# Performance work log

Measured on AMD Instinct MI355X. Metric: run time of the kernel, lower is better.

The kernel has to match this reference:

```python
import jax, jax.numpy as jnp
import numpy as np

APPERTURE = 256
Q_SCALE = 0.06


def setup_inputs() -> dict:
    key = jax.random.key(0)
    ks = jax.random.split(key, 5)
    B, N, D_IN, D_OUT = 4, 4096, 1024, 1024
    std = 1.0 / np.sqrt(D_IN)
    x = jax.random.normal(ks[0], (B, N, D_IN), dtype=jnp.float32)
    Wk = jax.random.normal(ks[1], (D_OUT, D_IN), dtype=jnp.float32) * std
    Wq = jax.random.normal(ks[2], (D_OUT, D_IN), dtype=jnp.float32) * std
    Wv = jax.random.normal(ks[3], (D_OUT, D_IN), dtype=jnp.float32) * std
    Wo = jax.random.normal(ks[4], (D_IN, D_OUT), dtype=jnp.float32) * std
    return {"x": x, "Wk": Wk, "Wq": Wq, "Wv": Wv, "Wo": Wo}


def reference(x, Wk, Wq, Wv, Wo):
    # x: [B, N, D_in]; torch Linear(W) computes x @ W.T
    K = jnp.einsum('bnd,od->bno', x, Wk)          # [B, N, D_out]
    Q = jnp.einsum('bnd,od->bno', x, Wq) * Q_SCALE
    V = jnp.einsum('bnd,od->bno', x, Wv)
    logits = jnp.einsum('bno,bmo->bnm', Q, K)      # [B, N, N]
    N = x.shape[1]
    idx = jnp.arange(N)
    # tril(-a) + triu(a) masks |i-j| >= apperture (keep strict band)
    band_mask = jnp.abs(idx[:, None] - idx[None, :]) >= APPERTURE  # [N, N]
    logits = jnp.where(band_mask[None, :, :], -jnp.inf, logits)
    att_weights = jax.nn.softmax(logits, axis=-1)  # [B, N, N]
    # dropout is identity in eval mode
    # y = (V^T @ weights)^T  ->  y[b,n,:] = sum_m att[b,m,n] * V[b,m,:]
    y = jnp.einsum('bmn,bmo->bno', att_weights, V)
    y = jnp.einsum('bno,io->bni', y, Wo)           # [B, N, D_in]
    return (y, att_weights)
```

## Files before the change

kernel.cpp:

```cpp
#include <hip/hip_runtime.h>
#include <stdint.h>

#define SEQ 4096
#define DM  1024
#define NB  4
#define QSCALE 0.06f

typedef __attribute__((ext_vector_type(8))) short short8;
typedef __attribute__((ext_vector_type(4))) float floatx4;

__device__ __forceinline__ unsigned short f2bf(float f) {
  union { float f; unsigned int u; } v; v.f = f;
  unsigned int u = v.u;
  u += 0x7FFFu + ((u >> 16) & 1u);
  return (unsigned short)(u >> 16);
}

__device__ __forceinline__ void async16(const void* g, void* l) {
  __builtin_amdgcn_global_load_lds(
      (const __attribute__((address_space(1))) void*)g,
      (__attribute__((address_space(3))) void*)l, 16, 0, 0);
}

__global__ void cvt_bf16(const float* __restrict__ in,
                         unsigned short* __restrict__ out, int n) {
  int i = (blockIdx.x * 256 + threadIdx.x) * 8;
  if (i >= n) return;
  const float4* p = (const float4*)(in + i);
  float4 a = p[0], b = p[1];
  short8 o;
  o[0] = (short)f2bf(a.x); o[1] = (short)f2bf(a.y);
  o[2] = (short)f2bf(a.z); o[3] = (short)f2bf(a.w);
  o[4] = (short)f2bf(b.x); o[5] = (short)f2bf(b.y);
  o[6] = (short)f2bf(b.z); o[7] = (short)f2bf(b.w);
  *(short8*)(out + i) = o;
}

template <bool OUT_BF16>
__global__ __launch_bounds__(256) void gemm_bt(
    const unsigned short* __restrict__ A, const unsigned short* __restrict__ W,
    void* __restrict__ Cout, float alpha, long ldc) {
  __shared__ unsigned short sA[128 * 32];
  __shared__ unsigned short sB[128 * 32];
  const int K = 1024;
  int tid = threadIdx.x;
  int wid = tid >> 6, lane = tid & 63;
  int wr = wid >> 1, wc = wid & 1;
  long rowBase = (long)blockIdx.x * 128;
  int colBase = blockIdx.y * 128;

  floatx4 acc[4][4];
#pragma unroll
  for (int i = 0; i < 4; i++)
#pragma unroll
    for (int j = 0; j < 4; j++) acc[i][j] = (floatx4){0.f, 0.f, 0.f, 0.f};

  int c0 = wid * 64 + lane;
  int c1 = c0 + 256;
  const unsigned short* Ag0 = A + (rowBase + (c0 >> 2)) * K + (c0 & 3) * 8;
  const unsigned short* Ag1 = A + (rowBase + (c1 >> 2)) * K + (c1 & 3) * 8;
  const unsigned short* Bg0 = W + ((long)colBase + (c0 >> 2)) * K + (c0 & 3) * 8;
  const unsigned short* Bg1 = W + ((long)colBase + (c1 >> 2)) * K + (c1 & 3) * 8;
  unsigned short* sA0 = sA + (wid * 64) * 8;
  unsigned short* sA1 = sA + (256 + wid * 64) * 8;
  unsigned short* sB0 = sB + (wid * 64) * 8;
  unsigned short* sB1 = sB + (256 + wid * 64) * 8;

  int aRd = (wr * 64 + (lane & 15)) * 32 + (lane >> 4) * 8;
  int bRd = (wc * 64 + (lane & 15)) * 32 + (lane >> 4) * 8;

  for (int ks = 0; ks < K; ks += 32) {
    async16(Ag0 + ks, sA0);
    async16(Ag1 + ks, sA1);
    async16(Bg0 + ks, sB0);
    async16(Bg1 + ks, sB1);
    __syncthreads();
    short8 af[4], bf[4];
#pragma unroll
    for (int mt = 0; mt < 4; mt++) af[mt] = *(const short8*)(sA + aRd + mt * 512);
#pragma unroll
    for (int nt = 0; nt < 4; nt++) bf[nt] = *(const short8*)(sB + bRd + nt * 512);
#pragma unroll
    for (int mt = 0; mt < 4; mt++)
#pragma unroll
      for (int nt = 0; nt < 4; nt++)
        acc[mt][nt] = __builtin_amdgcn_mfma_f32_16x16x32_bf16(
            af[mt], bf[nt], acc[mt][nt], 0, 0, 0);
    __syncthreads();
  }

  long crow = rowBase + wr * 64 + (lane >> 4) * 4;
  int ccol = colBase + wc * 64 + (lane & 15);
#pragma unroll
  for (int mt = 0; mt < 4; mt++)
#pragma unroll
    for (int nt = 0; nt < 4; nt++)
#pragma unroll
      for (int r = 0; r < 4; r++) {
        float v = acc[mt][nt][r] * alpha;
        long idx = (crow + mt * 16 + r) * ldc + ccol + nt * 16;
        if (OUT_BF16)
          ((unsigned short*)Cout)[idx] = f2bf(v);
        else
          ((float*)Cout)[idx] = v;
      }
}

__global__ __launch_bounds__(256) void attn_logits(
    const unsigned short* __restrict__ Qb, const unsigned short* __restrict__ Kb,
    float* __restrict__ att) {
  int b = blockIdx.z;
  int n0 = blockIdx.y * 128;
  int m0 = n0 - 256 + blockIdx.x * 128;
  if (m0 + 128 <= 0 || m0 >= SEQ) return;
  __shared__ unsigned short sA[128 * 32];
  __shared__ unsigned short sB[128 * 32];
  const int K = 1024;
  int tid = threadIdx.x;
  int wid = tid >> 6, lane = tid & 63;
  int wr = wid >> 1, wc = wid & 1;

  floatx4 acc[4][4];
#pragma unroll
  for (int i = 0; i < 4; i++)
#pragma unroll
    for (int j = 0; j < 4; j++) acc[i][j] = (floatx4){0.f, 0.f, 0.f, 0.f};

  int c0 = wid * 64 + lane;
  int c1 = c0 + 256;
  const unsigned short* Qbase = Qb + (long)b * SEQ * K;
  const unsigned short* Kbase = Kb + (long)b * SEQ * K;
  int br0 = m0 + (c0 >> 2); br0 = br0 < 0 ? 0 : (br0 > SEQ - 1 ? SEQ - 1 : br0);
  int br1 = m0 + (c1 >> 2); br1 = br1 < 0 ? 0 : (br1 > SEQ - 1 ? SEQ - 1 : br1);
  const unsigned short* Ag0 = Qbase + (long)(n0 + (c0 >> 2)) * K + (c0 & 3) * 8;
  const unsigned short* Ag1 = Qbase + (long)(n0 + (c1 >> 2)) * K + (c1 & 3) * 8;
  const unsigned short* Bg0 = Kbase + (long)br0 * K + (c0 & 3) * 8;
  const unsigned short* Bg1 = Kbase + (long)br1 * K + (c1 & 3) * 8;
  unsigned short* sA0 = sA + (wid * 64) * 8;
  unsigned short* sA1 = sA + (256 + wid * 64) * 8;
  unsigned short* sB0 = sB + (wid * 64) * 8;
  unsigned short* sB1 = sB + (256 + wid * 64) * 8;

  int aRd = (wr * 64 + (lane & 15)) * 32 + (lane >> 4) * 8;
  int bRd = (wc * 64 + (lane & 15)) * 32 + (lane >> 4) * 8;

  for (int ks = 0; ks < K; ks += 32) {
    async16(Ag0 + ks, sA0);
    async16(Ag1 + ks, sA1);
    async16(Bg0 + ks, sB0);
    async16(Bg1 + ks, sB1);
    __syncthreads();
    short8 af[4], bf[4];
#pragma unroll
    for (int mt = 0; mt < 4; mt++) af[mt] = *(const short8*)(sA + aRd + mt * 512);
#pragma unroll
    for (int nt = 0; nt < 4; nt++) bf[nt] = *(const short8*)(sB + bRd + nt * 512);
#pragma unroll
    for (int mt = 0; mt < 4; mt++)
#pragma unroll
      for (int nt = 0; nt < 4; nt++)
        acc[mt][nt] = __builtin_amdgcn_mfma_f32_16x16x32_bf16(
            af[mt], bf[nt], acc[mt][nt], 0, 0, 0);
    __syncthreads();
  }

  float* attB = att + (long)b * SEQ * SEQ;
  int crow = n0 + wr * 64 + (lane >> 4) * 4;
  int ccol = m0 + wc * 64 + (lane & 15);
#pragma unroll
  for (int mt = 0; mt < 4; mt++)
#pragma unroll
    for (int nt = 0; nt < 4; nt++)
#pragma unroll
      for (int r = 0; r < 4; r++) {
        int row = crow + mt * 16 + r;
        int col = ccol + nt * 16;
        int d = row - col;
        if (col >= 0 && col < SEQ && d < 256 && d > -256)
          attB[(long)row * SEQ + col] = acc[mt][nt][r];
      }
}

__global__ __launch_bounds__(256) void softmax_band(
    float* __restrict__ att, unsigned short* __restrict__ attT2) {
  __shared__ float e_lds[16 * 545];
  __shared__ float inv_s[16];
  int blk = blockIdx.x;
  int b = blk >> 8;
  int r0 = (blk & 255) * 16;
  int tid = threadIdx.x;
  int row = tid >> 4;
  int t16 = tid & 15;
  int i = r0 + row;
  int jbase = r0 - 272;
  float* arow = att + ((long)b * SEQ + i) * (long)SEQ;

  float raw[34];
  float m = -1e30f;
#pragma unroll
  for (int s = 0; s < 34; s++) {
    int jj = s * 16 + t16;
    int j = jbase + jj;
    bool ok = (j >= 0) && (j < SEQ) && (j >= i - 255) && (j <= i + 255);
    float v = ok ? arow[j] : -1e30f;
    raw[s] = v;
    m = fmaxf(m, v);
  }
#pragma unroll
  for (int off = 8; off; off >>= 1) m = fmaxf(m, __shfl_xor(m, off, 16));

  float sum = 0.f;
#pragma unroll
  for (int s = 0; s < 34; s++) {
    int jj = s * 16 + t16;
    float e = (raw[s] > -1e29f) ? __expf(raw[s] - m) : 0.f;
    e_lds[row * 545 + jj] = e;
    sum += e;
  }
#pragma unroll
  for (int off = 8; off; off >>= 1) sum += __shfl_xor(sum, off, 16);
  float invr = 1.0f / sum;
  if (t16 == 0) inv_s[row] = invr;
  __syncthreads();

  for (int s = 0; s < 64; s++) {
    int j0 = (s * 16 + t16) * 4;
    float4 w;
    float* wp = (float*)&w;
#pragma unroll
    for (int k = 0; k < 4; k++) {
      int j = j0 + k;
      bool ok = (j >= i - 255) && (j <= i + 255);
      int jj = j - jbase;
      jj = jj < 0 ? 0 : (jj > 543 ? 543 : jj);
      wp[k] = ok ? e_lds[row * 545 + jj] * invr : 0.f;
    }
    *(float4*)(arow + j0) = w;
  }

  int nn = tid >> 4;
  int mi16 = tid & 15;
  int i2 = r0 + mi16;
  float inv2 = inv_s[mi16];
  for (int s = 0; s <= 32; s++) {
    int n = r0 - 256 + s * 16 + nn;
    if (n < 0 || n >= SEQ) continue;
    int N0b = n & ~127;
    int mi = i2 - N0b + 256;
    if (mi < 0 || mi >= 640) continue;
    bool ok = (n >= i2 - 255) && (n <= i2 + 255);
    int jj = n - jbase;
    float val = ok ? e_lds[mi16 * 545 + jj] * inv2 : 0.f;
    attT2[(((long)b * 32 + (N0b >> 7)) * 128 + (n & 127)) * 640 + mi] = f2bf(val);
  }
}

__global__ __launch_bounds__(256) void attv_gemm(
    const unsigned short* __restrict__ attT2, const unsigned short* __restrict__ Vt,
    unsigned short* __restrict__ yb) {
  __shared__ unsigned short sA[128 * 32];
  __shared__ unsigned short sB[128 * 32];
  const int KA = 640;
  int b = blockIdx.z;
  int tid = threadIdx.x;
  int wid = tid >> 6, lane = tid & 63;
  int wr = wid >> 1, wc = wid & 1;
  int N0 = blockIdx.x * 128;
  int o0 = blockIdx.y * 128;

  floatx4 acc[4][4];
#pragma unroll
  for (int i = 0; i < 4; i++)
#pragma unroll
    for (int j = 0; j < 4; j++) acc[i][j] = (floatx4){0.f, 0.f, 0.f, 0.f};

  int c0 = wid * 64 + lane;
  int c1 = c0 + 256;
  const unsigned short* Abase =
      attT2 + (((long)b * 32 + blockIdx.x) * 128) * KA;
  const unsigned short* Ag0 = Abase + (long)(c0 >> 2) * KA + (c0 & 3) * 8;
  const unsigned short* Ag1 = Abase + (long)(c1 >> 2) * KA + (c1 & 3) * 8;
  const unsigned short* Bg0 = Vt + (long)(o0 + (c0 >> 2)) * (NB * SEQ) + (c0 & 3) * 8;
  const unsigned short* Bg1 = Vt + (long)(o0 + (c1 >> 2)) * (NB * SEQ) + (c1 & 3) * 8;
  unsigned short* sA0 = sA + (wid * 64) * 8;
  unsigned short* sA1 = sA + (256 + wid * 64) * 8;
  unsigned short* sB0 = sB + (wid * 64) * 8;
  unsigned short* sB1 = sB + (256 + wid * 64) * 8;

  int aRd = (wr * 64 + (lane & 15)) * 32 + (lane >> 4) * 8;
  int bRd = (wc * 64 + (lane & 15)) * 32 + (lane >> 4) * 8;

  for (int ks = 0; ks < KA; ks += 32) {
    int mg = N0 - 256 + ks;
    int mc = mg < 0 ? 0 : (mg > SEQ - 32 ? SEQ - 32 : mg);
    long boff = (long)b * SEQ + mc;
    async16(Ag0 + ks, sA0);
    async16(Ag1 + ks, sA1);
    async16(Bg0 + boff, sB0);
    async16(Bg1 + boff, sB1);
    __syncthreads();
    short8 af[4], bf[4];
#pragma unroll
    for (int mt = 0; mt < 4; mt++) af[mt] = *(const short8*)(sA + aRd + mt * 512);
#pragma unroll
    for (int nt = 0; nt < 4; nt++) bf[nt] = *(const short8*)(sB + bRd + nt * 512);
#pragma unroll
    for (int mt = 0; mt < 4; mt++)
#pragma unroll
      for (int nt = 0; nt < 4; nt++)
        acc[mt][nt] = __builtin_amdgcn_mfma_f32_16x16x32_bf16(
            af[mt], bf[nt], acc[mt][nt], 0, 0, 0);
    __syncthreads();
  }

  long crow = (long)b * SEQ + N0 + wr * 64 + (lane >> 4) * 4;
  int ccol = o0 + wc * 64 + (lane & 15);
#pragma unroll
  for (int mt = 0; mt < 4; mt++)
#pragma unroll
    for (int nt = 0; nt < 4; nt++)
#pragma unroll
      for (int r = 0; r < 4; r++)
        yb[(crow + mt * 16 + r) * DM + ccol + nt * 16] = f2bf(acc[mt][nt][r]);
}

extern "C" void kernel_launch(void* const* d_in, const int* in_sizes, int n_in,
                              void* d_out, int out_size, void* d_ws, size_t ws_size,
                              hipStream_t stream) {
  const float* x  = (const float*)d_in[0];
  const float* Wk = (const float*)d_in[1];
  const float* Wq = (const float*)d_in[2];
  const float* Wv = (const float*)d_in[3];
  const float* Wo = (const float*)d_in[4];
  float* outY = (float*)d_out;
  float* outAtt = outY + (long)NB * SEQ * DM;

  char* ws = (char*)d_ws;
  unsigned short* xb  = (unsigned short*)(ws + 0);
  unsigned short* Kb  = (unsigned short*)(ws + 33554432);
  unsigned short* Qb  = (unsigned short*)(ws + 67108864);
  unsigned short* Vt  = (unsigned short*)(ws + 100663296);
  unsigned short* Wkb = (unsigned short*)(ws + 134217728);
  unsigned short* Wqb = Wkb + 1048576;
  unsigned short* Wvb = Wqb + 1048576;
  unsigned short* Wob = Wvb + 1048576;
  unsigned short* attT2 = Kb;
  unsigned short* yb = xb;

  cvt_bf16<<<8192, 256, 0, stream>>>(x, xb, NB * SEQ * DM);
  cvt_bf16<<<512, 256, 0, stream>>>(Wk, Wkb, DM * DM);
  cvt_bf16<<<512, 256, 0, stream>>>(Wq, Wqb, DM * DM);
  cvt_bf16<<<512, 256, 0, stream>>>(Wv, Wvb, DM * DM);
  cvt_bf16<<<512, 256, 0, stream>>>(Wo, Wob, DM * DM);

  dim3 gg(128, 8);
  gemm_bt<true><<<gg, 256, 0, stream>>>(xb, Wkb, Kb, 1.0f, 1024);
  gemm_bt<true><<<gg, 256, 0, stream>>>(xb, Wqb, Qb, QSCALE, 1024);
  gemm_bt<true><<<dim3(8, 128), 256, 0, stream>>>(Wvb, xb, Vt, 1.0f, NB * SEQ);

  attn_logits<<<dim3(5, 32, NB), 256, 0, stream>>>(Qb, Kb, outAtt);
  hipMemsetAsync(attT2, 0, (size_t)NB * 32 * 128 * 640 * 2, stream);
  softmax_band<<<1024, 256, 0, stream>>>(outAtt, attT2);
  attv_gemm<<<dim3(32, 8, NB), 256, 0, stream>>>(attT2, Vt, yb);
  gemm_bt<false><<<gg, 256, 0, stream>>>(yb, Wob, outY, 1.0f, 1024);
}
```

Measured before the change: 736.1 us.

## Replace projection GEMMs with 256x256-tile, 4-stage pipelined 512-thread kernel

Replaces the 128x128 single-buffered projection GEMM with a 256x256 tile kernel using 8 waves and a 4-deep LDS ring buffer. Async global-to-LDS loads are issued three K-steps ahead and interleaved with MFMA phases, with raised wave priority during compute. Block index swizzling is added to improve L2 locality. This targets the exposed load latency and barrier stalls of the old loop, at the cost of 128KB of LDS per block and more accumulator registers, which may limit occupancy. The grid shrinks to 256 blocks, roughly one per CU.

```diff
diff --git a/kernel.cpp b/kernel.cpp
--- a/kernel.cpp
+++ b/kernel.cpp
@@ -36,63 +36,108 @@
   *(short8*)(out + i) = o;
 }
 
-template <bool OUT_BF16>
-__global__ __launch_bounds__(256) void gemm_bt(
+template <bool OUT_BF16, int MT>
+__global__ __launch_bounds__(512, 2) void gemm256(
     const unsigned short* __restrict__ A, const unsigned short* __restrict__ W,
     void* __restrict__ Cout, float alpha, long ldc) {
-  __shared__ unsigned short sA[128 * 32];
-  __shared__ unsigned short sB[128 * 32];
+  __shared__ __align__(16) unsigned short lds[4 * 16384];
   const int K = 1024;
+  const int NKT = 32;
   int tid = threadIdx.x;
-  int wid = tid >> 6, lane = tid & 63;
-  int wr = wid >> 1, wc = wid & 1;
-  long rowBase = (long)blockIdx.x * 128;
-  int colBase = blockIdx.y * 128;
-
-  floatx4 acc[4][4];
-#pragma unroll
-  for (int i = 0; i < 4; i++)
+  int lane = tid & 63;
+  int wid = tid >> 6;
+  int wr = wid >> 2, wc = wid & 3;
+
+  int bid = blockIdx.x;
+  int raw = ((bid & 7) << 5) | (bid >> 3);
+  int bx = raw % MT;
+  int by = raw / MT;
+  long brow = (long)bx * 256;
+  long bcol = (long)by * 256;
+
+  floatx4 acc[8][4];
+#pragma unroll
+  for (int i = 0; i < 8; i++)
 #pragma unroll
     for (int j = 0; j < 4; j++) acc[i][j] = (floatx4){0.f, 0.f, 0.f, 0.f};
 
-  int c0 = wid * 64 + lane;
-  int c1 = c0 + 256;
-  const unsigned short* Ag0 = A + (rowBase + (c0 >> 2)) * K + (c0 & 3) * 8;
-  const unsigned short* Ag1 = A + (rowBase + (c1 >> 2)) * K + (c1 & 3) * 8;
-  const unsigned short* Bg0 = W + ((long)colBase + (c0 >> 2)) * K + (c0 & 3) * 8;
-  const unsigned short* Bg1 = W + ((long)colBase + (c1 >> 2)) * K + (c1 & 3) * 8;
-  unsigned short* sA0 = sA + (wid * 64) * 8;
-  unsigned short* sA1 = sA + (256 + wid * 64) * 8;
-  unsigned short* sB0 = sB + (wid * 64) * 8;
-  unsigned short* sB1 = sB + (256 + wid * 64) * 8;
-
-  int aRd = (wr * 64 + (lane & 15)) * 32 + (lane >> 4) * 8;
+  const unsigned short* Ag = A + (brow + (tid >> 2)) * K + (tid & 3) * 8;
+  const unsigned short* Wg = W + (bcol + (tid >> 2)) * K + (tid & 3) * 8;
+  unsigned short* ldsW = lds + wid * 512;
+
+  int aRd = (wr * 128 + (lane & 15)) * 32 + (lane >> 4) * 8;
   int bRd = (wc * 64 + (lane & 15)) * 32 + (lane >> 4) * 8;
 
-  for (int ks = 0; ks < K; ks += 32) {
-    async16(Ag0 + ks, sA0);
-    async16(Ag1 + ks, sA1);
-    async16(Bg0 + ks, sB0);
-    async16(Bg1 + ks, sB1);
-    __syncthreads();
-    short8 af[4], bf[4];
-#pragma unroll
-    for (int mt = 0; mt < 4; mt++) af[mt] = *(const short8*)(sA + aRd + mt * 512);
-#pragma unroll
-    for (int nt = 0; nt < 4; nt++) bf[nt] = *(const short8*)(sB + bRd + nt * 512);
+#pragma unroll
+  for (int tt = 0; tt < 3; tt++) {
+    unsigned short* d = ldsW + tt * 16384;
+    const unsigned short* a = Ag + tt * 32;
+    const unsigned short* w = Wg + tt * 32;
+    async16(a, d);
+    async16(a + 128 * K, d + 4096);
+    async16(w, d + 8192);
+    async16(w + 128 * K, d + 12288);
+  }
+  asm volatile("s_waitcnt vmcnt(8)" ::: "memory");
+  __builtin_amdgcn_s_barrier();
+
+  for (int t = 0; t < NKT; ++t) {
+    const unsigned short* bufA = lds + (t & 3) * 16384;
+    const unsigned short* bufB = bufA + 8192;
+    short8 a0[4], b0[4], a1[4];
+#pragma unroll
+    for (int mt = 0; mt < 4; mt++)
+      a0[mt] = *(const short8*)(bufA + aRd + mt * 512);
+#pragma unroll
+    for (int nt = 0; nt < 4; nt++)
+      b0[nt] = *(const short8*)(bufB + bRd + nt * 512);
+    if (t + 3 < NKT) {
+      unsigned short* d = ldsW + ((t + 3) & 3) * 16384;
+      const unsigned short* a = Ag + (t + 3) * 32;
+      async16(a, d);
+      async16(a + 128 * K, d + 4096);
+    }
+    __builtin_amdgcn_s_barrier();
+    __builtin_amdgcn_s_setprio(1);
 #pragma unroll
     for (int mt = 0; mt < 4; mt++)
 #pragma unroll
       for (int nt = 0; nt < 4; nt++)
         acc[mt][nt] = __builtin_amdgcn_mfma_f32_16x16x32_bf16(
-            af[mt], bf[nt], acc[mt][nt], 0, 0, 0);
-    __syncthreads();
-  }
-
-  long crow = rowBase + wr * 64 + (lane >> 4) * 4;
-  int ccol = colBase + wc * 64 + (lane & 15);
-#pragma unroll
-  for (int mt = 0; mt < 4; mt++)
+            a0[mt], b0[nt], acc[mt][nt], 0, 0, 0);
+    __builtin_amdgcn_s_setprio(0);
+    __builtin_amdgcn_s_barrier();
+#pragma unroll
+    for (int mt = 0; mt < 4; mt++)
+      a1[mt] = *(const short8*)(bufA + aRd + 2048 + mt * 512);
+    if (t + 3 < NKT) {
+      unsigned short* d = ldsW + ((t + 3) & 3) * 16384;
+      const unsigned short* w = Wg + (t + 3) * 32;
+      async16(w, d + 8192);
+      async16(w + 128 * K, d + 12288);
+    }
+    __builtin_amdgcn_s_barrier();
+    __builtin_amdgcn_s_setprio(1);
+#pragma unroll
+    for (int mt = 0; mt < 4; mt++)
+#pragma unroll
+      for (int nt = 0; nt < 4; nt++)
+        acc[4 + mt][nt] = __builtin_amdgcn_mfma_f32_16x16x32_bf16(
+            a1[mt], b0[nt], acc[4 + mt][nt], 0, 0, 0);
+    __builtin_amdgcn_s_setprio(0);
+    if (t < NKT - 3)
+      asm volatile("s_waitcnt vmcnt(8)" ::: "memory");
+    else if (t == NKT - 3)
+      asm volatile("s_waitcnt vmcnt(4)" ::: "memory");
+    else
+      asm volatile("s_waitcnt vmcnt(0)" ::: "memory");
+    __builtin_amdgcn_s_barrier();
+  }
+
+  long crow = brow + wr * 128 + (lane >> 4) * 4;
+  long ccol = bcol + wc * 64 + (lane & 15);
+#pragma unroll
+  for (int mt = 0; mt < 8; mt++)
 #pragma unroll
     for (int nt = 0; nt < 4; nt++)
 #pragma unroll
@@ -353,14 +398,13 @@
   cvt_bf16<<<512, 256, 0, stream>>>(Wv, Wvb, DM * DM);
   cvt_bf16<<<512, 256, 0, stream>>>(Wo, Wob, DM * DM);
 
-  dim3 gg(128, 8);
-  gemm_bt<true><<<gg, 256, 0, stream>>>(xb, Wkb, Kb, 1.0f, 1024);
-  gemm_bt<true><<<gg, 256, 0, stream>>>(xb, Wqb, Qb, QSCALE, 1024);
-  gemm_bt<true><<<dim3(8, 128), 256, 0, stream>>>(Wvb, xb, Vt, 1.0f, NB * SEQ);
+  gemm256<true, 64><<<256, 512, 0, stream>>>(xb, Wkb, Kb, 1.0f, 1024);
+  gemm256<true, 64><<<256, 512, 0, stream>>>(xb, Wqb, Qb, QSCALE, 1024);
+  gemm256<true, 4><<<256, 512, 0, stream>>>(Wvb, xb, Vt, 1.0f, NB * SEQ);
 
   attn_logits<<<dim3(5, 32, NB), 256, 0, stream>>>(Qb, Kb, outAtt);
   hipMemsetAsync(attT2, 0, (size_t)NB * 32 * 128 * 640 * 2, stream);
   softmax_band<<<1024, 256, 0, stream>>>(outAtt, attT2);
   attv_gemm<<<dim3(32, 8, NB), 256, 0, stream>>>(attT2, Vt, yb);
-  gemm_bt<false><<<gg, 256, 0, stream>>>(yb, Wob, outY, 1.0f, 1024);
-}
+  gemm256<false, 64><<<256, 512, 0, stream>>>(yb, Wob, outY, 1.0f, 1024);
+}
```

Result: faster. 688.7 us (-6.4%).
